# Optimization experiments

Hardware: AMD Instinct MI355X
Metric: run time of the kernel (lower is better)

The kernel has to match this reference:

```python
import jax, jax.numpy as jnp
import numpy as np

INPUT_SIZE, HIDDEN, N, T = 124, 64, 4096, 64


def setup_inputs() -> dict:
    key = jax.random.key(0)
    ks = jax.random.split(key, 12)
    s = 1.0 / np.sqrt(HIDDEN)  # PyTorch RNN init: U(-1/sqrt(h), 1/sqrt(h))
    u = lambda k, shape: jax.random.uniform(k, shape, jnp.float32, -s, s)
    return {
        "x": jax.random.normal(ks[0], (N, T, INPUT_SIZE), jnp.float32),
        "W_ih0": u(ks[1], (HIDDEN, INPUT_SIZE)),
        "W_hh0": u(ks[2], (HIDDEN, HIDDEN)),
        "b_ih0": u(ks[3], (HIDDEN,)),
        "b_hh0": u(ks[4], (HIDDEN,)),
        "W_ih1": u(ks[5], (HIDDEN, HIDDEN)),
        "W_hh1": u(ks[6], (HIDDEN, HIDDEN)),
        "b_ih1": u(ks[7], (HIDDEN,)),
        "b_hh1": u(ks[8], (HIDDEN,)),
        "W_fc": u(ks[9], (1, HIDDEN)),
        "b_fc": u(ks[10], (1,)),
    }


def reference(x, W_ih0, W_hh0, b_ih0, b_hh0, W_ih1, W_hh1, b_ih1, b_hh1, W_fc, b_fc):
    # 2-layer tanh RNN (batch_first), eval mode (dropout inactive).
    # Precompute layer-0 input projections for all timesteps: [T, N, H]
    xproj = jnp.einsum("ntf,hf->tnh", x, W_ih0) + b_ih0
    h0 = jnp.zeros((x.shape[0], HIDDEN), x.dtype)
    h1 = jnp.zeros((x.shape[0], HIDDEN), x.dtype)

    def step(carry, xp_t):
        h0, h1 = carry
        h0 = jnp.tanh(xp_t + h0 @ W_hh0.T + b_hh0)
        h1 = jnp.tanh(h0 @ W_ih1.T + b_ih1 + h1 @ W_hh1.T + b_hh1)
        return (h0, h1), None

    (h0, h1), _ = jax.lax.scan(step, (h0, h1), xproj)
    # out[:, -1, :] of top layer == final h1; linear head to scalar
    return (h1 @ W_fc.T + b_fc).squeeze(-1)  # [N]
```

## Files before the change

### kernel.cpp

```cpp
#include <hip/hip_runtime.h>
#include <hip/hip_bf16.h>
#include <stdint.h>


typedef float  f32x4 __attribute__((ext_vector_type(4)));
typedef short  s16x8 __attribute__((ext_vector_type(8)));
typedef unsigned int u32;

#define TSTEPS 64
#define FIN    124
#define HID    64

__device__ __forceinline__ f32x4 zero4() {
  f32x4 z = {0.f, 0.f, 0.f, 0.f};
  return z;
}

__device__ __forceinline__ void barrier_lds() {
  asm volatile("s_waitcnt lgkmcnt(0)" ::: "memory");
  __builtin_amdgcn_s_barrier();
  asm volatile("" ::: "memory");
}

__device__ __forceinline__ void split8(const f32x4 a, const f32x4 b,
                                       s16x8& hi, s16x8& lo) {
  float e[8] = {a[0], a[1], a[2], a[3], b[0], b[1], b[2], b[3]};
  s16x8 h, l;
#pragma unroll
  for (int p = 0; p < 8; ++p) {
    float v = e[p];
    __hip_bfloat16 bh = __float2bfloat16(v);
    float r = v - __bfloat162float(bh);
    __hip_bfloat16 bl = __float2bfloat16(r);
    h[p] = (short)__builtin_bit_cast(unsigned short, bh);
    l[p] = (short)__builtin_bit_cast(unsigned short, bl);
  }
  hi = h;
  lo = l;
}

__device__ __forceinline__ f32x4 MFMA(s16x8 a, s16x8 b, f32x4 c) {
  return __builtin_amdgcn_mfma_f32_16x16x32_bf16(a, b, c, 0, 0, 0);
}

__device__ __forceinline__ float tanh_f(float x) {
  float e = __builtin_amdgcn_exp2f(x * 2.885390081777927f);
  return __builtin_fmaf(-2.f, __builtin_amdgcn_rcpf(e + 1.f), 1.f);
}

__global__ __launch_bounds__(256, 1) void rnn2_fused_kernel(
    const float* __restrict__ x,
    const float* __restrict__ Wih0, const float* __restrict__ Whh0,
    const float* __restrict__ bih0, const float* __restrict__ bhh0,
    const float* __restrict__ Wih1, const float* __restrict__ Whh1,
    const float* __restrict__ bih1, const float* __restrict__ bhh1,
    const float* __restrict__ Wfc,  const float* __restrict__ bfc,
    float* __restrict__ out) {
  __shared__ __align__(16) unsigned short XH[2][16][136];
  __shared__ __align__(16) unsigned short XL[2][16][136];
  __shared__ __align__(16) unsigned short S0H[2][16][72];
  __shared__ __align__(16) unsigned short S0L[2][16][72];
  __shared__ __align__(16) unsigned short S1H[2][16][72];
  __shared__ __align__(16) unsigned short S1L[2][16][72];
  __shared__ float WFC[64];
  __shared__ float RED[64];

  const int tid  = (int)threadIdx.x;
  const int lane = tid & 63;
  const int wv   = tid >> 6;
  const int r16  = lane & 15;
  const int g    = lane >> 4;
  const int col  = 16 * wv + r16;
  const int n0   = (int)blockIdx.x * 16;

  s16x8 WH[3][2][2];
  {
    const float* Wp[3] = {Whh0, Wih1, Whh1};
#pragma unroll
    for (int p = 0; p < 3; ++p) {
#pragma unroll
      for (int c = 0; c < 2; ++c) {
        const float* base = Wp[p] + col * HID + 32 * c + 8 * g;
        f32x4 a = *(const f32x4*)base;
        f32x4 b = *(const f32x4*)(base + 4);
        split8(a, b, WH[p][c][0], WH[p][c][1]);
      }
    }
  }
  s16x8 WI[4][2];
#pragma unroll
  for (int c = 0; c < 4; ++c) {
    const float* base = Wih0 + col * FIN + 32 * c + 8 * g;
    f32x4 a = *(const f32x4*)base;
    f32x4 b = zero4();
    if (!(c == 3 && g == 3)) b = *(const f32x4*)(base + 4);
    split8(a, b, WI[c][0], WI[c][1]);
  }

  const float bias0 = bih0[col] + bhh0[col];
  const float bias1 = bih1[col] + bhh1[col];

  {
    u32* z0 = (u32*)&S0H[0][0][0];
    u32* z1 = (u32*)&S0L[0][0][0];
    u32* z2 = (u32*)&S1H[0][0][0];
    u32* z3 = (u32*)&S1L[0][0][0];
    for (int i = tid; i < 16 * 72 / 2; i += 256) {
      z0[i] = 0; z1[i] = 0; z2[i] = 0; z3[i] = 0;
    }
  }
  if (tid < 64) WFC[tid] = Wfc[tid];

  const int xr = tid >> 4;
  const int xs = tid & 15;
  const float* xrow = x + (size_t)(n0 + xr) * (TSTEPS * FIN);
  f32x4 xa, xb;
  {
    const float* b0 = xrow + 8 * xs;
    xa = *(const f32x4*)b0;
    xb = zero4();
    if (xs != 15) xb = *(const f32x4*)(b0 + 4);
    s16x8 fh, fl;
    split8(xa, xb, fh, fl);
    *(s16x8*)&XH[0][xr][8 * xs] = fh;
    *(s16x8*)&XL[0][xr][8 * xs] = fl;
  }
  {
    const float* b1 = xrow + FIN + 8 * xs;
    xa = *(const f32x4*)b1;
    xb = zero4();
    if (xs != 15) xb = *(const f32x4*)(b1 + 4);
  }
  barrier_lds();

#pragma unroll 2
  for (int t = 0; t < TSTEPS; ++t) {
    const int P = t & 1;

    {
      s16x8 fh, fl;
      split8(xa, xb, fh, fl);
      *(s16x8*)&XH[1 - P][xr][8 * xs] = fh;
      *(s16x8*)&XL[1 - P][xr][8 * xs] = fl;
    }
    {
      int t2 = (t + 2 < TSTEPS) ? (t + 2) : (TSTEPS - 1);
      const float* bp = xrow + t2 * FIN + 8 * xs;
      xa = *(const f32x4*)bp;
      xb = zero4();
      if (xs != 15) xb = *(const f32x4*)(bp + 4);
    }

    s16x8 h0h[2], h0l[2], xh[4], xl[4], h1h[2], h1l[2];
#pragma unroll
    for (int c = 0; c < 2; ++c) {
      h0h[c] = *(const s16x8*)&S0H[P][r16][32 * c + 8 * g];
      h0l[c] = *(const s16x8*)&S0L[P][r16][32 * c + 8 * g];
      h1h[c] = *(const s16x8*)&S1H[P][r16][32 * c + 8 * g];
      h1l[c] = *(const s16x8*)&S1L[P][r16][32 * c + 8 * g];
    }
#pragma unroll
    for (int c = 0; c < 4; ++c) {
      xh[c] = *(const s16x8*)&XH[P][r16][32 * c + 8 * g];
      xl[c] = *(const s16x8*)&XL[P][r16][32 * c + 8 * g];
    }

    f32x4 a0 = {bias0, bias0, bias0, bias0};
    f32x4 a1 = zero4();
    f32x4 a2 = zero4();
    f32x4 a3 = zero4();
    f32x4 a4 = zero4();
    f32x4 a5 = zero4();
    f32x4 b0 = {bias1, bias1, bias1, bias1};
    f32x4 b1 = zero4();

    a0 = MFMA(h0h[0], WH[0][0][0], a0);
    a1 = MFMA(h0h[0], WH[0][0][1], a1);
    a2 = MFMA(h0l[0], WH[0][0][0], a2);
    a3 = MFMA(xh[2], WI[2][0], a3);
    a4 = MFMA(xh[2], WI[2][1], a4);
    a5 = MFMA(xl[2], WI[2][0], a5);
    b0 = MFMA(h1h[0], WH[2][0][0], b0);
    b1 = MFMA(h1l[0], WH[2][0][0], b1);

    a0 = MFMA(h0h[1], WH[0][1][0], a0);
    a1 = MFMA(h0h[1], WH[0][1][1], a1);
    a2 = MFMA(h0l[1], WH[0][1][0], a2);
    a3 = MFMA(xh[3], WI[3][0], a3);
    a4 = MFMA(xh[3], WI[3][1], a4);
    a5 = MFMA(xl[3], WI[3][0], a5);
    b0 = MFMA(h1h[1], WH[2][1][0], b0);
    b1 = MFMA(h1l[1], WH[2][1][0], b1);

    a0 = MFMA(xh[0], WI[0][0], a0);
    a1 = MFMA(xh[0], WI[0][1], a1);
    a2 = MFMA(xl[0], WI[0][0], a2);
    b0 = MFMA(h1h[0], WH[2][0][1], b0);

    a0 = MFMA(xh[1], WI[1][0], a0);
    a1 = MFMA(xh[1], WI[1][1], a1);
    a2 = MFMA(xl[1], WI[1][0], a2);
    b0 = MFMA(h1h[1], WH[2][1][1], b0);

#pragma unroll
    for (int i = 0; i < 4; ++i) {
      float h = tanh_f(((a0[i] + a1[i]) + (a2[i] + a3[i])) + (a4[i] + a5[i]));
      __hip_bfloat16 bh = __float2bfloat16(h);
      float rl = h - __bfloat162float(bh);
      __hip_bfloat16 bl = __float2bfloat16(rl);
      S0H[1 - P][4 * g + i][col] = __builtin_bit_cast(unsigned short, bh);
      S0L[1 - P][4 * g + i][col] = __builtin_bit_cast(unsigned short, bl);
    }
    barrier_lds();

    f32x4 b2 = zero4();
    f32x4 b3 = zero4();
#pragma unroll
    for (int c = 0; c < 2; ++c) {
      s16x8 ah = *(const s16x8*)&S0H[1 - P][r16][32 * c + 8 * g];
      s16x8 al = *(const s16x8*)&S0L[1 - P][r16][32 * c + 8 * g];
      b2 = MFMA(ah, WH[1][c][0], b2);
      b3 = MFMA(al, WH[1][c][0], b3);
      b2 = MFMA(ah, WH[1][c][1], b2);
    }
#pragma unroll
    for (int i = 0; i < 4; ++i) {
      float h = tanh_f((b0[i] + b1[i]) + (b2[i] + b3[i]));
      __hip_bfloat16 bh = __float2bfloat16(h);
      float rl = h - __bfloat162float(bh);
      __hip_bfloat16 bl = __float2bfloat16(rl);
      S1H[1 - P][4 * g + i][col] = __builtin_bit_cast(unsigned short, bh);
      S1L[1 - P][4 * g + i][col] = __builtin_bit_cast(unsigned short, bl);
    }
    barrier_lds();
  }

  if (tid < 64) {
    const int r = tid & 15;
    const int q = tid >> 4;
    float acc = 0.f;
#pragma unroll
    for (int k = 0; k < 16; ++k) {
      int kk = 16 * q + k;
      float hv = __uint_as_float(((u32)S1H[0][r][kk]) << 16) +
                 __uint_as_float(((u32)S1L[0][r][kk]) << 16);
      acc += hv * WFC[kk];
    }
    RED[tid] = acc;
  }
  barrier_lds();
  if (tid < 16) {
    float o = RED[tid] + RED[tid + 16] + RED[tid + 32] + RED[tid + 48] + bfc[0];
    out[n0 + tid] = o;
  }
}

extern "C" void kernel_launch(void* const* d_in, const int* in_sizes, int n_in,
                              void* d_out, int out_size, void* d_ws,
                              size_t ws_size, hipStream_t stream) {
  (void)in_sizes; (void)n_in; (void)d_ws; (void)ws_size; (void)out_size;
  const float* x    = (const float*)d_in[0];
  const float* Wih0 = (const float*)d_in[1];
  const float* Whh0 = (const float*)d_in[2];
  const float* bih0 = (const float*)d_in[3];
  const float* bhh0 = (const float*)d_in[4];
  const float* Wih1 = (const float*)d_in[5];
  const float* Whh1 = (const float*)d_in[6];
  const float* bih1 = (const float*)d_in[7];
  const float* bhh1 = (const float*)d_in[8];
  const float* Wfc  = (const float*)d_in[9];
  const float* bfc  = (const float*)d_in[10];

  rnn2_fused_kernel<<<256, 256, 0, stream>>>(
      x, Wih0, Whh0, bih0, bhh0, Wih1, Whh1, bih1, bhh1, Wfc, bfc,
      (float*)d_out);
}
```

Measured before the change: 222.4 us.

## Split layers across warp groups and pipeline layer 1 one step behind layer 0

Doubles the block to 512 threads. Waves 0-3 compute layer 0 for step s while waves 4-7 compute layer 1 for step s-1 and stage the next x tile. This cuts the per-step barrier count from two to one and runs the two layers' MFMA chains concurrently on the wavefront. The cost is twice the threads per block, an extra loop iteration to drain the pipeline, and a sequence that depends on correct double-buffer indexing of S1.

```diff
diff --git a/kernel.cpp b/kernel.cpp
--- a/kernel.cpp
+++ b/kernel.cpp
@@ -48,7 +48,7 @@
   return __builtin_fmaf(-2.f, __builtin_amdgcn_rcpf(e + 1.f), 1.f);
 }
 
-__global__ __launch_bounds__(256, 1) void rnn2_fused_kernel(
+__global__ __launch_bounds__(512, 2) void rnn2_fused_kernel(
     const float* __restrict__ x,
     const float* __restrict__ Wih0, const float* __restrict__ Whh0,
     const float* __restrict__ bih0, const float* __restrict__ bhh0,
@@ -68,54 +68,61 @@
   const int tid  = (int)threadIdx.x;
   const int lane = tid & 63;
   const int wv   = tid >> 6;
+  const bool L0  = (wv < 4);
   const int r16  = lane & 15;
   const int g    = lane >> 4;
-  const int col  = 16 * wv + r16;
+  const int col  = 16 * (wv & 3) + r16;
   const int n0   = (int)blockIdx.x * 16;
 
-  s16x8 WH[3][2][2];
-  {
-    const float* Wp[3] = {Whh0, Wih1, Whh1};
-#pragma unroll
-    for (int p = 0; p < 3; ++p) {
-#pragma unroll
-      for (int c = 0; c < 2; ++c) {
-        const float* base = Wp[p] + col * HID + 32 * c + 8 * g;
-        f32x4 a = *(const f32x4*)base;
-        f32x4 b = *(const f32x4*)(base + 4);
-        split8(a, b, WH[p][c][0], WH[p][c][1]);
-      }
-    }
-  }
-  s16x8 WI[4][2];
-#pragma unroll
-  for (int c = 0; c < 4; ++c) {
-    const float* base = Wih0 + col * FIN + 32 * c + 8 * g;
-    f32x4 a = *(const f32x4*)base;
-    f32x4 b = zero4();
-    if (!(c == 3 && g == 3)) b = *(const f32x4*)(base + 4);
-    split8(a, b, WI[c][0], WI[c][1]);
-  }
-
-  const float bias0 = bih0[col] + bhh0[col];
-  const float bias1 = bih1[col] + bhh1[col];
+  s16x8 WA[4][2];
+  s16x8 WB[2][2];
+  float bias;
+  if (L0) {
+#pragma unroll
+    for (int c = 0; c < 4; ++c) {
+      const float* base = Wih0 + col * FIN + 32 * c + 8 * g;
+      f32x4 a = *(const f32x4*)base;
+      f32x4 b = zero4();
+      if (!(c == 3 && g == 3)) b = *(const f32x4*)(base + 4);
+      split8(a, b, WA[c][0], WA[c][1]);
+    }
+#pragma unroll
+    for (int c = 0; c < 2; ++c) {
+      const float* base = Whh0 + col * HID + 32 * c + 8 * g;
+      split8(*(const f32x4*)base, *(const f32x4*)(base + 4),
+             WB[c][0], WB[c][1]);
+    }
+    bias = bih0[col] + bhh0[col];
+  } else {
+#pragma unroll
+    for (int c = 0; c < 2; ++c) {
+      const float* base = Wih1 + col * HID + 32 * c + 8 * g;
+      split8(*(const f32x4*)base, *(const f32x4*)(base + 4),
+             WA[c][0], WA[c][1]);
+      const float* base2 = Whh1 + col * HID + 32 * c + 8 * g;
+      split8(*(const f32x4*)base2, *(const f32x4*)(base2 + 4),
+             WA[2 + c][0], WA[2 + c][1]);
+    }
+    bias = bih1[col] + bhh1[col];
+  }
 
   {
     u32* z0 = (u32*)&S0H[0][0][0];
     u32* z1 = (u32*)&S0L[0][0][0];
     u32* z2 = (u32*)&S1H[0][0][0];
     u32* z3 = (u32*)&S1L[0][0][0];
-    for (int i = tid; i < 16 * 72 / 2; i += 256) {
+    for (int i = tid; i < 16 * 72 / 2; i += 512) {
       z0[i] = 0; z1[i] = 0; z2[i] = 0; z3[i] = 0;
     }
   }
   if (tid < 64) WFC[tid] = Wfc[tid];
 
-  const int xr = tid >> 4;
-  const int xs = tid & 15;
-  const float* xrow = x + (size_t)(n0 + xr) * (TSTEPS * FIN);
+  const int sidx = tid - 256;
+  const int xr = sidx >> 4;
+  const int xs = sidx & 15;
+  const float* xrow = x + (size_t)(n0 + (L0 ? 0 : xr)) * (TSTEPS * FIN);
   f32x4 xa, xb;
-  {
+  if (!L0) {
     const float* b0 = xrow + 8 * xs;
     xa = *(const f32x4*)b0;
     xb = zero4();
@@ -124,8 +131,6 @@
     split8(xa, xb, fh, fl);
     *(s16x8*)&XH[0][xr][8 * xs] = fh;
     *(s16x8*)&XL[0][xr][8 * xs] = fl;
-  }
-  {
     const float* b1 = xrow + FIN + 8 * xs;
     xa = *(const f32x4*)b1;
     xb = zero4();
@@ -134,103 +139,99 @@
   barrier_lds();
 
 #pragma unroll 2
-  for (int t = 0; t < TSTEPS; ++t) {
-    const int P = t & 1;
-
-    {
-      s16x8 fh, fl;
-      split8(xa, xb, fh, fl);
-      *(s16x8*)&XH[1 - P][xr][8 * xs] = fh;
-      *(s16x8*)&XL[1 - P][xr][8 * xs] = fl;
-    }
-    {
-      int t2 = (t + 2 < TSTEPS) ? (t + 2) : (TSTEPS - 1);
-      const float* bp = xrow + t2 * FIN + 8 * xs;
-      xa = *(const f32x4*)bp;
-      xb = zero4();
-      if (xs != 15) xb = *(const f32x4*)(bp + 4);
-    }
-
-    s16x8 h0h[2], h0l[2], xh[4], xl[4], h1h[2], h1l[2];
-#pragma unroll
-    for (int c = 0; c < 2; ++c) {
-      h0h[c] = *(const s16x8*)&S0H[P][r16][32 * c + 8 * g];
-      h0l[c] = *(const s16x8*)&S0L[P][r16][32 * c + 8 * g];
-      h1h[c] = *(const s16x8*)&S1H[P][r16][32 * c + 8 * g];
-      h1l[c] = *(const s16x8*)&S1L[P][r16][32 * c + 8 * g];
-    }
-#pragma unroll
-    for (int c = 0; c < 4; ++c) {
-      xh[c] = *(const s16x8*)&XH[P][r16][32 * c + 8 * g];
-      xl[c] = *(const s16x8*)&XL[P][r16][32 * c + 8 * g];
-    }
-
-    f32x4 a0 = {bias0, bias0, bias0, bias0};
-    f32x4 a1 = zero4();
-    f32x4 a2 = zero4();
-    f32x4 a3 = zero4();
-    f32x4 a4 = zero4();
-    f32x4 a5 = zero4();
-    f32x4 b0 = {bias1, bias1, bias1, bias1};
-    f32x4 b1 = zero4();
-
-    a0 = MFMA(h0h[0], WH[0][0][0], a0);
-    a1 = MFMA(h0h[0], WH[0][0][1], a1);
-    a2 = MFMA(h0l[0], WH[0][0][0], a2);
-    a3 = MFMA(xh[2], WI[2][0], a3);
-    a4 = MFMA(xh[2], WI[2][1], a4);
-    a5 = MFMA(xl[2], WI[2][0], a5);
-    b0 = MFMA(h1h[0], WH[2][0][0], b0);
-    b1 = MFMA(h1l[0], WH[2][0][0], b1);
-
-    a0 = MFMA(h0h[1], WH[0][1][0], a0);
-    a1 = MFMA(h0h[1], WH[0][1][1], a1);
-    a2 = MFMA(h0l[1], WH[0][1][0], a2);
-    a3 = MFMA(xh[3], WI[3][0], a3);
-    a4 = MFMA(xh[3], WI[3][1], a4);
-    a5 = MFMA(xl[3], WI[3][0], a5);
-    b0 = MFMA(h1h[1], WH[2][1][0], b0);
-    b1 = MFMA(h1l[1], WH[2][1][0], b1);
-
-    a0 = MFMA(xh[0], WI[0][0], a0);
-    a1 = MFMA(xh[0], WI[0][1], a1);
-    a2 = MFMA(xl[0], WI[0][0], a2);
-    b0 = MFMA(h1h[0], WH[2][0][1], b0);
-
-    a0 = MFMA(xh[1], WI[1][0], a0);
-    a1 = MFMA(xh[1], WI[1][1], a1);
-    a2 = MFMA(xl[1], WI[1][0], a2);
-    b0 = MFMA(h1h[1], WH[2][1][1], b0);
-
-#pragma unroll
-    for (int i = 0; i < 4; ++i) {
-      float h = tanh_f(((a0[i] + a1[i]) + (a2[i] + a3[i])) + (a4[i] + a5[i]));
-      __hip_bfloat16 bh = __float2bfloat16(h);
-      float rl = h - __bfloat162float(bh);
-      __hip_bfloat16 bl = __float2bfloat16(rl);
-      S0H[1 - P][4 * g + i][col] = __builtin_bit_cast(unsigned short, bh);
-      S0L[1 - P][4 * g + i][col] = __builtin_bit_cast(unsigned short, bl);
-    }
-    barrier_lds();
-
-    f32x4 b2 = zero4();
-    f32x4 b3 = zero4();
-#pragma unroll
-    for (int c = 0; c < 2; ++c) {
-      s16x8 ah = *(const s16x8*)&S0H[1 - P][r16][32 * c + 8 * g];
-      s16x8 al = *(const s16x8*)&S0L[1 - P][r16][32 * c + 8 * g];
-      b2 = MFMA(ah, WH[1][c][0], b2);
-      b3 = MFMA(al, WH[1][c][0], b3);
-      b2 = MFMA(ah, WH[1][c][1], b2);
-    }
-#pragma unroll
-    for (int i = 0; i < 4; ++i) {
-      float h = tanh_f((b0[i] + b1[i]) + (b2[i] + b3[i]));
-      __hip_bfloat16 bh = __float2bfloat16(h);
-      float rl = h - __bfloat162float(bh);
-      __hip_bfloat16 bl = __float2bfloat16(rl);
-      S1H[1 - P][4 * g + i][col] = __builtin_bit_cast(unsigned short, bh);
-      S1L[1 - P][4 * g + i][col] = __builtin_bit_cast(unsigned short, bl);
+  for (int s = 0; s <= TSTEPS; ++s) {
+    const int P = s & 1;
+
+    if (L0) {
+      if (s < TSTEPS) {
+        s16x8 hh[2], hl[2], xh[4], xl[4];
+#pragma unroll
+        for (int c = 0; c < 2; ++c) {
+          hh[c] = *(const s16x8*)&S0H[P][r16][32 * c + 8 * g];
+          hl[c] = *(const s16x8*)&S0L[P][r16][32 * c + 8 * g];
+        }
+#pragma unroll
+        for (int c = 0; c < 4; ++c) {
+          xh[c] = *(const s16x8*)&XH[P][r16][32 * c + 8 * g];
+          xl[c] = *(const s16x8*)&XL[P][r16][32 * c + 8 * g];
+        }
+        f32x4 a0 = {bias, bias, bias, bias};
+        f32x4 a1 = zero4(), a2 = zero4(), a3 = zero4(),
+              a4 = zero4(), a5 = zero4();
+        a0 = MFMA(hh[0], WB[0][0], a0);
+        a1 = MFMA(hh[0], WB[0][1], a1);
+        a2 = MFMA(hl[0], WB[0][0], a2);
+        a3 = MFMA(xh[1], WA[1][0], a3);
+        a4 = MFMA(xh[1], WA[1][1], a4);
+        a5 = MFMA(xl[1], WA[1][0], a5);
+        a0 = MFMA(hh[1], WB[1][0], a0);
+        a1 = MFMA(hh[1], WB[1][1], a1);
+        a2 = MFMA(hl[1], WB[1][0], a2);
+        a3 = MFMA(xh[2], WA[2][0], a3);
+        a4 = MFMA(xh[2], WA[2][1], a4);
+        a5 = MFMA(xl[2], WA[2][0], a5);
+        a0 = MFMA(xh[0], WA[0][0], a0);
+        a1 = MFMA(xh[0], WA[0][1], a1);
+        a2 = MFMA(xl[0], WA[0][0], a2);
+        a3 = MFMA(xh[3], WA[3][0], a3);
+        a4 = MFMA(xh[3], WA[3][1], a4);
+        a5 = MFMA(xl[3], WA[3][0], a5);
+#pragma unroll
+        for (int i = 0; i < 4; ++i) {
+          float h = tanh_f(((a0[i] + a1[i]) + (a2[i] + a3[i])) +
+                           (a4[i] + a5[i]));
+          __hip_bfloat16 bh = __float2bfloat16(h);
+          float rl = h - __bfloat162float(bh);
+          __hip_bfloat16 bl = __float2bfloat16(rl);
+          S0H[1 - P][4 * g + i][col] = __builtin_bit_cast(unsigned short, bh);
+          S0L[1 - P][4 * g + i][col] = __builtin_bit_cast(unsigned short, bl);
+        }
+      }
+    } else {
+      if (s < TSTEPS - 1) {
+        s16x8 fh, fl;
+        split8(xa, xb, fh, fl);
+        *(s16x8*)&XH[1 - P][xr][8 * xs] = fh;
+        *(s16x8*)&XL[1 - P][xr][8 * xs] = fl;
+        int t2 = (s + 2 < TSTEPS) ? (s + 2) : (TSTEPS - 1);
+        const float* bp = xrow + t2 * FIN + 8 * xs;
+        xa = *(const f32x4*)bp;
+        xb = zero4();
+        if (xs != 15) xb = *(const f32x4*)(bp + 4);
+      }
+      if (s >= 1) {
+        s16x8 gh[2], gl[2], qh[2], ql[2];
+#pragma unroll
+        for (int c = 0; c < 2; ++c) {
+          gh[c] = *(const s16x8*)&S0H[P][r16][32 * c + 8 * g];
+          gl[c] = *(const s16x8*)&S0L[P][r16][32 * c + 8 * g];
+          qh[c] = *(const s16x8*)&S1H[1 - P][r16][32 * c + 8 * g];
+          ql[c] = *(const s16x8*)&S1L[1 - P][r16][32 * c + 8 * g];
+        }
+        f32x4 b0 = {bias, bias, bias, bias};
+        f32x4 b1 = zero4(), b2 = zero4(), b3 = zero4();
+        b0 = MFMA(gh[0], WA[0][0], b0);
+        b1 = MFMA(gh[0], WA[0][1], b1);
+        b2 = MFMA(gl[0], WA[0][0], b2);
+        b3 = MFMA(ql[0], WA[2][0], b3);
+        b0 = MFMA(gh[1], WA[1][0], b0);
+        b1 = MFMA(gh[1], WA[1][1], b1);
+        b2 = MFMA(gl[1], WA[1][0], b2);
+        b3 = MFMA(ql[1], WA[3][0], b3);
+        b0 = MFMA(qh[0], WA[2][0], b0);
+        b1 = MFMA(qh[1], WA[3][0], b1);
+        b2 = MFMA(qh[0], WA[2][1], b2);
+        b3 = MFMA(qh[1], WA[3][1], b3);
+#pragma unroll
+        for (int i = 0; i < 4; ++i) {
+          float h = tanh_f((b0[i] + b1[i]) + (b2[i] + b3[i]));
+          __hip_bfloat16 bh = __float2bfloat16(h);
+          float rl = h - __bfloat162float(bh);
+          __hip_bfloat16 bl = __float2bfloat16(rl);
+          S1H[P][4 * g + i][col] = __builtin_bit_cast(unsigned short, bh);
+          S1L[P][4 * g + i][col] = __builtin_bit_cast(unsigned short, bl);
+        }
+      }
     }
     barrier_lds();
   }
@@ -250,7 +251,8 @@
   }
   barrier_lds();
   if (tid < 16) {
-    float o = RED[tid] + RED[tid + 16] + RED[tid + 32] + RED[tid + 48] + bfc[0];
+    float o = RED[tid] + RED[tid + 16] + RED[tid + 32] + RED[tid + 48] +
+              bfc[0];
     out[n0 + tid] = o;
   }
 }
@@ -271,7 +273,7 @@
   const float* Wfc  = (const float*)d_in[9];
   const float* bfc  = (const float*)d_in[10];
 
-  rnn2_fused_kernel<<<256, 256, 0, stream>>>(
+  rnn2_fused_kernel<<<256, 512, 0, stream>>>(
       x, Wih0, Whh0, bih0, bhh0, Wih1, Whh1, bih1, bhh1, Wfc, bfc,
       (float*)d_out);
 }
```

Result: no change. 220.2 us (-1.0%).
